# Kernel tuning notes

Measured on AMD Instinct MI355X. Metric: run time of the kernel, lower is better.

## Reference

```python
import jax, jax.numpy as jnp
import numpy as np

N_NODES = 50000
N_EDGES = 600000
IN_DIM = 128
OUT_DIM = 1024


def setup_inputs() -> dict:
    key = jax.random.key(0)
    k1, k2, k3 = jax.random.split(key, 3)
    x = jax.random.normal(k1, (N_NODES, IN_DIM), dtype=jnp.float32)
    edge_index = jax.random.randint(k2, (2, N_EDGES), 0, N_NODES, dtype=jnp.int64)
    # Linear(3*in_dim, out_dim): weight stored as [3*in_dim, out_dim] for x @ W
    W = jax.random.normal(k3, (3 * IN_DIM, OUT_DIM), dtype=jnp.float32) * (1.0 / np.sqrt(3 * IN_DIM))
    b = jnp.zeros((OUT_DIM,), dtype=jnp.float32)
    return {"x": x, "edge_index": edge_index, "W": W, "b": b}


def _mean_aggregate(feats, seg_ids, n):
    # segment-mean: sum gathered features per segment, divide by count (>=1)
    s = jax.ops.segment_sum(feats, seg_ids, num_segments=n)          # [N, d]
    cnt = jax.ops.segment_sum(jnp.ones((feats.shape[0],), feats.dtype), seg_ids, num_segments=n)
    return s / jnp.maximum(cnt, 1.0)[:, None]


def reference(x, edge_index, W, b):
    n = x.shape[0]
    src = edge_index[0]
    dst = edge_index[1]
    # mean over in-neighbors (messages flow src -> dst)
    mean_in = _mean_aggregate(x[src], dst, n)
    # mean over out-neighbors (messages flow dst -> src)
    mean_out = _mean_aggregate(x[dst], src, n)
    h = jnp.concatenate([x, mean_in, mean_out], axis=-1)             # [N, 3*in_dim]
    return jax.nn.relu(h @ W + b)                                    # [N, out_dim]
```

## Files before the change

kernel.cpp:

```cpp
#include <hip/hip_runtime.h>
#include <hip/hip_bf16.h>


typedef __attribute__((ext_vector_type(8))) short bf16x8;
typedef __attribute__((ext_vector_type(4))) short bf16x4;
typedef __attribute__((ext_vector_type(4))) float f32x4;

#define IN_DIM 128
#define AGG 256
#define K3 384
#define ODIM 1024

static __device__ inline short bfs(float f) {
    union { __hip_bfloat16 b; short s; } u;
    u.b = __float2bfloat16(f);
    return u.s;
}

static __device__ inline float bf2f(short s) {
    union { unsigned u; float f; } c;
    c.u = ((unsigned)(unsigned short)s) << 16;
    return c.f;
}

__global__ __launch_bounds__(256) void sage_prep(
    const float* __restrict__ x, const int* __restrict__ src,
    const int* __restrict__ dst, const float* __restrict__ W,
    __hip_bfloat16* __restrict__ xb, __hip_bfloat16* __restrict__ Wt,
    int* __restrict__ deg, int* __restrict__ pos,
    int n_nodes, int n_edges, int wtB, int convB)
{
    int b = blockIdx.x;
    int t = threadIdx.x;
    if (b < wtB) {
        __shared__ __hip_bfloat16 lds[32][36];
        int tk = b / 32, tn = b % 32;
        int k0 = tk * 32, n0 = tn * 32;
        int r = t >> 3, c = (t & 7) * 4;
        f32x4 w = *(const f32x4*)(W + (size_t)(k0 + r) * ODIM + n0 + c);
#pragma unroll
        for (int i = 0; i < 4; ++i) lds[c + i][r] = __float2bfloat16(w[i]);
        __syncthreads();
        *(bf16x4*)&Wt[(size_t)(n0 + r) * K3 + k0 + c] = *(bf16x4*)&lds[r][c];
        return;
    }
    b -= wtB;
    if (b < convB) {
        int tid = b * 256 + t;
        if (tid >= n_nodes * 16) return;
        int i = tid >> 4, d8 = (tid & 15) << 3;
        const float* xp = x + (size_t)i * IN_DIM + d8;
        f32x4 a = *(const f32x4*)xp;
        f32x4 c4 = *(const f32x4*)(xp + 4);
        bf16x8 v;
        v[0] = bfs(a.x); v[1] = bfs(a.y); v[2] = bfs(a.z); v[3] = bfs(a.w);
        v[4] = bfs(c4.x); v[5] = bfs(c4.y); v[6] = bfs(c4.z); v[7] = bfs(c4.w);
        *(bf16x8*)(xb + (size_t)i * IN_DIM + d8) = v;
        return;
    }
    b -= convB;
    int e = b * 256 + t;
    if (e >= 2 * n_edges) return;
    int idx = (e < n_edges) ? dst[e] : n_nodes + src[e - n_edges];
    pos[e] = atomicAdd(deg + idx, 1);
}

__global__ __launch_bounds__(256) void scan_partial(
    const int* __restrict__ deg, int* __restrict__ off, int* __restrict__ bsum, int n)
{
    __shared__ int s[256];
    int t = threadIdx.x;
    int base = blockIdx.x * 1024 + t * 4;
    int4 v = {0, 0, 0, 0};
    if (base + 3 < n) v = *(const int4*)(deg + base);
    else {
        if (base     < n) v.x = deg[base];
        if (base + 1 < n) v.y = deg[base + 1];
        if (base + 2 < n) v.z = deg[base + 2];
        if (base + 3 < n) v.w = deg[base + 3];
    }
    int tsum = v.x + v.y + v.z + v.w;
    s[t] = tsum;
    __syncthreads();
#pragma unroll
    for (int d = 1; d < 256; d <<= 1) {
        int add = (t >= d) ? s[t - d] : 0;
        __syncthreads();
        s[t] += add;
        __syncthreads();
    }
    int excl = s[t] - tsum;
    if (t == 255) bsum[blockIdx.x] = s[255];
    int e0 = excl, e1 = e0 + v.x, e2 = e1 + v.y, e3 = e2 + v.z;
    if (base     < n) off[base]     = e0;
    if (base + 1 < n) off[base + 1] = e1;
    if (base + 2 < n) off[base + 2] = e2;
    if (base + 3 < n) off[base + 3] = e3;
}

__global__ __launch_bounds__(256) void scan_add(
    int* __restrict__ off, const int* __restrict__ bsum, int n, int nblk)
{
    __shared__ int s[256];
    int t = threadIdx.x;
    int v = (t < nblk) ? bsum[t] : 0;
    s[t] = v;
    __syncthreads();
#pragma unroll
    for (int d = 1; d < 256; d <<= 1) {
        int add = (t >= d) ? s[t - d] : 0;
        __syncthreads();
        s[t] += add;
        __syncthreads();
    }
    int b = s[blockIdx.x] - ((blockIdx.x < nblk) ? bsum[blockIdx.x] : 0);
    int base = blockIdx.x * 1024 + t * 4;
#pragma unroll
    for (int j = 0; j < 4; ++j)
        if (base + j < n) off[base + j] += b;
}

__global__ __launch_bounds__(256) void sage_fill(
    const int* __restrict__ src, const int* __restrict__ dst,
    const int* __restrict__ off, const int* __restrict__ pos,
    int* __restrict__ csr, int n_nodes, int n_edges)
{
    int t = blockIdx.x * 256 + threadIdx.x;
    if (t >= 2 * n_edges) return;
    int node, val;
    if (t < n_edges) { node = dst[t]; val = src[t]; }
    else { int e = t - n_edges; node = n_nodes + src[e]; val = dst[e]; }
    csr[off[node] + pos[t]] = val;
}

__global__ __launch_bounds__(256) void sage_aggregate(
    const __hip_bfloat16* __restrict__ xb, const int* __restrict__ csr,
    const int* __restrict__ off, const int* __restrict__ deg,
    __hip_bfloat16* __restrict__ hagg, int n_nodes)
{
    int wid  = (int)((blockIdx.x * 256 + threadIdx.x) >> 6);
    int lane = threadIdx.x & 63;
    if (wid >= 2 * n_nodes) return;
    int i = wid >> 1;
    int d = wid & 1;
    int idx = i + d * n_nodes;

    int b0 = off[idx], dg = deg[idx];
    const int* cp = csr + b0;
    int q = lane >> 4, sub = lane & 15;

    float acc[8];
#pragma unroll
    for (int j = 0; j < 8; ++j) acc[j] = 0.f;

#define ACC8(v) { _Pragma("unroll") \
    for (int j = 0; j < 8; ++j) acc[j] += bf2f((v)[j]); }

    int e = 0;
    for (; e + 7 < dg; e += 8) {
        int r0 = cp[e + q];
        int r1 = cp[e + 4 + q];
        bf16x8 v0 = *(const bf16x8*)(xb + (size_t)r0 * IN_DIM + sub * 8);
        bf16x8 v1 = *(const bf16x8*)(xb + (size_t)r1 * IN_DIM + sub * 8);
        ACC8(v0) ACC8(v1)
    }
    for (; e < dg; e += 4) {
        int eq = e + q;
        int rq = cp[min(eq, dg - 1)];
        bf16x8 v = *(const bf16x8*)(xb + (size_t)rq * IN_DIM + sub * 8);
        if (eq < dg) ACC8(v)
    }
#undef ACC8

#pragma unroll
    for (int j = 0; j < 8; ++j) {
        acc[j] += __shfl_xor(acc[j], 16);
        acc[j] += __shfl_xor(acc[j], 32);
    }

    float inv = 1.0f / (float)max(dg, 1);
    if (q == 0) {
        bf16x8 o;
#pragma unroll
        for (int j = 0; j < 8; ++j) o[j] = bfs(acc[j] * inv);
        *(bf16x8*)(hagg + (size_t)i * AGG + d * IN_DIM + sub * 8) = o;
    }
}

__global__ __launch_bounds__(256, 4) void sage_gemm(
    const __hip_bfloat16* __restrict__ xb, const __hip_bfloat16* __restrict__ hagg,
    const __hip_bfloat16* __restrict__ Wt, const float* __restrict__ bias,
    float* __restrict__ out, int n_nodes)
{
    __shared__ __hip_bfloat16 Asm[2][128 * 32];
    __shared__ __hip_bfloat16 Bsm[2][128 * 32];

    int t    = threadIdx.x;
    int wave = t >> 6;
    int lane = t & 63;

    int bid = blockIdx.x;
    int sid = bid;
    if ((gridDim.x & 7) == 0) {
        int cpx = gridDim.x >> 3;
        sid = (bid & 7) * cpx + (bid >> 3);
    }
    int tn   = sid & 7;
    int tm   = sid >> 3;
    int m0   = tm * 128;
    int n0   = tn * 128;
    int wm   = wave >> 1;
    int wn   = wave & 1;
    int m    = lane & 15;
    int quad = lane >> 4;

    int srow = t >> 2;
    int seg  = t & 3;
    int g    = seg ^ (srow & 3);
    int ga0  = m0 + srow;       if (ga0 >= n_nodes) ga0 = n_nodes - 1;
    int ga1  = m0 + srow + 64;  if (ga1 >= n_nodes) ga1 = n_nodes - 1;
    const __hip_bfloat16* xA0 = xb   + (size_t)ga0 * IN_DIM + g * 8;
    const __hip_bfloat16* xA1 = xb   + (size_t)ga1 * IN_DIM + g * 8;
    const __hip_bfloat16* hA0 = hagg + (size_t)ga0 * AGG    + g * 8;
    const __hip_bfloat16* hA1 = hagg + (size_t)ga1 * AGG    + g * 8;
    const __hip_bfloat16* gB0 = Wt + (size_t)(n0 + srow) * K3 + g * 8;
    const __hip_bfloat16* gB1 = Wt + (size_t)(n0 + srow + 64) * K3 + g * 8;
    int l0 = (0 * 256 + wave * 64) * 8;
    int l1 = (1 * 256 + wave * 64) * 8;

    f32x4 acc[4][4];
#pragma unroll
    for (int s = 0; s < 4; ++s)
#pragma unroll
        for (int u = 0; u < 4; ++u) acc[s][u] = (f32x4){0.f, 0.f, 0.f, 0.f};

    __builtin_amdgcn_global_load_lds(xA0, &Asm[0][l0], 16, 0, 0);
    __builtin_amdgcn_global_load_lds(xA1, &Asm[0][l1], 16, 0, 0);
    __builtin_amdgcn_global_load_lds(gB0, &Bsm[0][l0], 16, 0, 0);
    __builtin_amdgcn_global_load_lds(gB1, &Bsm[0][l1], 16, 0, 0);

    int slot = quad ^ (m & 3);
#pragma unroll
    for (int kt = 0; kt < 12; ++kt) {
        int p = kt & 1;
        __syncthreads();
        if (kt < 11) {
            int kn = kt + 1;
            const __hip_bfloat16* pA0 = (kn < 4) ? xA0 + kn * 32 : hA0 + (kn - 4) * 32;
            const __hip_bfloat16* pA1 = (kn < 4) ? xA1 + kn * 32 : hA1 + (kn - 4) * 32;
            __builtin_amdgcn_global_load_lds(pA0, &Asm[p ^ 1][l0], 16, 0, 0);
            __builtin_amdgcn_global_load_lds(pA1, &Asm[p ^ 1][l1], 16, 0, 0);
            __builtin_amdgcn_global_load_lds(gB0 + kn * 32, &Bsm[p ^ 1][l0], 16, 0, 0);
            __builtin_amdgcn_global_load_lds(gB1 + kn * 32, &Bsm[p ^ 1][l1], 16, 0, 0);
        }
        bf16x8 a[4], b[4];
#pragma unroll
        for (int s = 0; s < 4; ++s) {
            int row = wm * 64 + s * 16 + m;
            a[s] = *(const bf16x8*)&Asm[p][row * 32 + slot * 8];
        }
#pragma unroll
        for (int u = 0; u < 4; ++u) {
            int row = wn * 64 + u * 16 + m;
            b[u] = *(const bf16x8*)&Bsm[p][row * 32 + slot * 8];
        }
#pragma unroll
        for (int s = 0; s < 4; ++s)
#pragma unroll
            for (int u = 0; u < 4; ++u)
                acc[s][u] = __builtin_amdgcn_mfma_f32_16x16x32_bf16(a[s], b[u], acc[s][u], 0, 0, 0);
    }

    float bv[4];
#pragma unroll
    for (int u = 0; u < 4; ++u) bv[u] = bias[n0 + wn * 64 + u * 16 + m];

    bool full = (m0 + 128 <= n_nodes);
    if (full) {
#pragma unroll
        for (int s = 0; s < 4; ++s) {
            int r0 = m0 + wm * 64 + s * 16 + quad * 4;
#pragma unroll
            for (int r = 0; r < 4; ++r) {
                float* orow = out + (size_t)(r0 + r) * ODIM + n0 + wn * 64 + m;
#pragma unroll
                for (int u = 0; u < 4; ++u)
                    __builtin_nontemporal_store(fmaxf(acc[s][u][r] + bv[u], 0.f), orow + u * 16);
            }
        }
    } else {
#pragma unroll
        for (int s = 0; s < 4; ++s) {
            int r0 = m0 + wm * 64 + s * 16 + quad * 4;
#pragma unroll
            for (int r = 0; r < 4; ++r) {
                if (r0 + r >= n_nodes) continue;
                float* orow = out + (size_t)(r0 + r) * ODIM + n0 + wn * 64 + m;
#pragma unroll
                for (int u = 0; u < 4; ++u)
                    __builtin_nontemporal_store(fmaxf(acc[s][u][r] + bv[u], 0.f), orow + u * 16);
            }
        }
    }
}

extern "C" void kernel_launch(void* const* d_in, const int* in_sizes, int n_in,
                              void* d_out, int out_size, void* d_ws, size_t ws_size,
                              hipStream_t stream)
{
    const float* x    = (const float*)d_in[0];
    const int*   ei   = (const int*)d_in[1];
    const float* W    = (const float*)d_in[2];
    const float* bias = (const float*)d_in[3];

    int n_nodes = in_sizes[0] / IN_DIM;
    int n_edges = in_sizes[1] / 2;
    const int* src = ei;
    const int* dst = ei + n_edges;
    int n2 = 2 * n_nodes;

    char* ws = (char*)d_ws;
    int* deg  = (int*)ws;
    int* off  = deg + n2;
    int* bsum = off + n2;
    int* pos  = bsum + 256;
    int* csr  = pos + 2 * n_edges;
    __hip_bfloat16* hagg = (__hip_bfloat16*)(csr + 2 * n_edges);
    __hip_bfloat16* Wt   = hagg + (size_t)n_nodes * AGG;
    __hip_bfloat16* xb   = Wt + (size_t)K3 * ODIM;

    hipMemsetAsync(deg, 0, (size_t)n2 * sizeof(int), stream);

    int wtB   = (K3 / 32) * (ODIM / 32);
    int convB = (n_nodes * 16 + 255) / 256;
    int degB  = (2 * n_edges + 255) / 256;
    sage_prep<<<wtB + convB + degB, 256, 0, stream>>>(
        x, src, dst, W, xb, Wt, deg, pos, n_nodes, n_edges, wtB, convB);

    int nblk = (n2 + 1023) / 1024;
    scan_partial<<<nblk, 256, 0, stream>>>(deg, off, bsum, n2);
    scan_add<<<nblk, 256, 0, stream>>>(off, bsum, n2, nblk);

    sage_fill<<<degB, 256, 0, stream>>>(src, dst, off, pos, csr, n_nodes, n_edges);

    sage_aggregate<<<(n2 + 3) / 4, 256, 0, stream>>>(xb, csr, off, deg, hagg, n_nodes);

    int tiles_m = (n_nodes + 127) / 128;
    int blocks  = tiles_m * (ODIM / 128);
    sage_gemm<<<blocks, 256, 0, stream>>>(xb, hagg, Wt, bias, (float*)d_out, n_nodes);
}
```

Measured before the change: 397.7 us.

## Fuse CSR build stages into one cooperative kernel with grid syncs

Replaces the memset, prep, two scan kernels and fill kernel with a single cooperative persistent kernel of 1024 blocks that uses grid-wide syncs between phases. The goal is to remove several kernel launch gaps and the separate memset. In exchange, the grid-stride loops run fewer blocks than before, and each grid.sync has its own cost. Occupancy is limited by the cooperative launch and the launch bounds.

```diff
diff --git a/kernel.cpp b/kernel.cpp
--- a/kernel.cpp
+++ b/kernel.cpp
@@ -1,5 +1,8 @@
 #include <hip/hip_runtime.h>
 #include <hip/hip_bf16.h>
+#include <hip/hip_cooperative_groups.h>
+
+namespace cg = cooperative_groups;
 
 
 typedef __attribute__((ext_vector_type(8))) short bf16x8;
@@ -10,6 +13,7 @@
 #define AGG 256
 #define K3 384
 #define ODIM 1024
+#define MEGA_NB 1024
 
 static __device__ inline short bfs(float f) {
     union { __hip_bfloat16 b; short s; } u;
@@ -23,114 +27,117 @@
     return c.f;
 }
 
-__global__ __launch_bounds__(256) void sage_prep(
+__global__ __launch_bounds__(256, 4) void sage_mega(
     const float* __restrict__ x, const int* __restrict__ src,
     const int* __restrict__ dst, const float* __restrict__ W,
     __hip_bfloat16* __restrict__ xb, __hip_bfloat16* __restrict__ Wt,
-    int* __restrict__ deg, int* __restrict__ pos,
-    int n_nodes, int n_edges, int wtB, int convB)
+    int* __restrict__ deg, int* __restrict__ pos, int* __restrict__ off,
+    int* __restrict__ bsum, int* __restrict__ csr,
+    int n_nodes, int n_edges, int wtB, int convB, int nblk)
 {
-    int b = blockIdx.x;
-    int t = threadIdx.x;
-    if (b < wtB) {
-        __shared__ __hip_bfloat16 lds[32][36];
-        int tk = b / 32, tn = b % 32;
-        int k0 = tk * 32, n0 = tn * 32;
-        int r = t >> 3, c = (t & 7) * 4;
-        f32x4 w = *(const f32x4*)(W + (size_t)(k0 + r) * ODIM + n0 + c);
-#pragma unroll
-        for (int i = 0; i < 4; ++i) lds[c + i][r] = __float2bfloat16(w[i]);
-        __syncthreads();
-        *(bf16x4*)&Wt[(size_t)(n0 + r) * K3 + k0 + c] = *(bf16x4*)&lds[r][c];
-        return;
-    }
-    b -= wtB;
-    if (b < convB) {
-        int tid = b * 256 + t;
-        if (tid >= n_nodes * 16) return;
-        int i = tid >> 4, d8 = (tid & 15) << 3;
-        const float* xp = x + (size_t)i * IN_DIM + d8;
-        f32x4 a = *(const f32x4*)xp;
-        f32x4 c4 = *(const f32x4*)(xp + 4);
-        bf16x8 v;
-        v[0] = bfs(a.x); v[1] = bfs(a.y); v[2] = bfs(a.z); v[3] = bfs(a.w);
-        v[4] = bfs(c4.x); v[5] = bfs(c4.y); v[6] = bfs(c4.z); v[7] = bfs(c4.w);
-        *(bf16x8*)(xb + (size_t)i * IN_DIM + d8) = v;
-        return;
-    }
-    b -= convB;
-    int e = b * 256 + t;
-    if (e >= 2 * n_edges) return;
-    int idx = (e < n_edges) ? dst[e] : n_nodes + src[e - n_edges];
-    pos[e] = atomicAdd(deg + idx, 1);
-}
-
-__global__ __launch_bounds__(256) void scan_partial(
-    const int* __restrict__ deg, int* __restrict__ off, int* __restrict__ bsum, int n)
-{
-    __shared__ int s[256];
-    int t = threadIdx.x;
-    int base = blockIdx.x * 1024 + t * 4;
-    int4 v = {0, 0, 0, 0};
-    if (base + 3 < n) v = *(const int4*)(deg + base);
-    else {
-        if (base     < n) v.x = deg[base];
-        if (base + 1 < n) v.y = deg[base + 1];
-        if (base + 2 < n) v.z = deg[base + 2];
-        if (base + 3 < n) v.w = deg[base + 3];
-    }
-    int tsum = v.x + v.y + v.z + v.w;
-    s[t] = tsum;
-    __syncthreads();
-#pragma unroll
-    for (int d = 1; d < 256; d <<= 1) {
-        int add = (t >= d) ? s[t - d] : 0;
-        __syncthreads();
-        s[t] += add;
-        __syncthreads();
-    }
-    int excl = s[t] - tsum;
-    if (t == 255) bsum[blockIdx.x] = s[255];
-    int e0 = excl, e1 = e0 + v.x, e2 = e1 + v.y, e3 = e2 + v.z;
-    if (base     < n) off[base]     = e0;
-    if (base + 1 < n) off[base + 1] = e1;
-    if (base + 2 < n) off[base + 2] = e2;
-    if (base + 3 < n) off[base + 3] = e3;
-}
-
-__global__ __launch_bounds__(256) void scan_add(
-    int* __restrict__ off, const int* __restrict__ bsum, int n, int nblk)
-{
-    __shared__ int s[256];
-    int t = threadIdx.x;
-    int v = (t < nblk) ? bsum[t] : 0;
-    s[t] = v;
-    __syncthreads();
-#pragma unroll
-    for (int d = 1; d < 256; d <<= 1) {
-        int add = (t >= d) ? s[t - d] : 0;
-        __syncthreads();
-        s[t] += add;
-        __syncthreads();
-    }
-    int b = s[blockIdx.x] - ((blockIdx.x < nblk) ? bsum[blockIdx.x] : 0);
-    int base = blockIdx.x * 1024 + t * 4;
-#pragma unroll
-    for (int j = 0; j < 4; ++j)
-        if (base + j < n) off[base + j] += b;
-}
-
-__global__ __launch_bounds__(256) void sage_fill(
-    const int* __restrict__ src, const int* __restrict__ dst,
-    const int* __restrict__ off, const int* __restrict__ pos,
-    int* __restrict__ csr, int n_nodes, int n_edges)
-{
-    int t = blockIdx.x * 256 + threadIdx.x;
-    if (t >= 2 * n_edges) return;
-    int node, val;
-    if (t < n_edges) { node = dst[t]; val = src[t]; }
-    else { int e = t - n_edges; node = n_nodes + src[e]; val = dst[e]; }
-    csr[off[node] + pos[t]] = val;
+    cg::grid_group grid = cg::this_grid();
+    __shared__ short wtl[32][36];
+    __shared__ int ss[256];
+    const int NB = (int)gridDim.x;
+    const int t  = threadIdx.x;
+    const int n2 = 2 * n_nodes;
+    const int E2 = 2 * n_edges;
+
+    for (int i = blockIdx.x * 256 + t; i < n2; i += NB * 256) deg[i] = 0;
+    grid.sync();
+
+    int degB = (E2 + 255) >> 8;
+    int totB = wtB + convB + degB;
+    for (int j = blockIdx.x; j < totB; j += NB) {
+        if (j < wtB) {
+            int tk = j / 32, tn = j - tk * 32;
+            int k0 = tk * 32, n0 = tn * 32;
+            int r = t >> 3, c = (t & 7) * 4;
+            f32x4 w = *(const f32x4*)(W + (size_t)(k0 + r) * ODIM + n0 + c);
+#pragma unroll
+            for (int i2 = 0; i2 < 4; ++i2) wtl[c + i2][r] = bfs(w[i2]);
+            __syncthreads();
+            *(bf16x4*)&Wt[(size_t)(n0 + r) * K3 + k0 + c] = *(bf16x4*)&wtl[r][c];
+            __syncthreads();
+        } else if (j < wtB + convB) {
+            int tid = (j - wtB) * 256 + t;
+            if (tid < n_nodes * 16) {
+                int i = tid >> 4, d8 = (tid & 15) << 3;
+                const float* xp = x + (size_t)i * IN_DIM + d8;
+                f32x4 a = *(const f32x4*)xp;
+                f32x4 c4 = *(const f32x4*)(xp + 4);
+                bf16x8 v;
+                v[0] = bfs(a.x); v[1] = bfs(a.y); v[2] = bfs(a.z); v[3] = bfs(a.w);
+                v[4] = bfs(c4.x); v[5] = bfs(c4.y); v[6] = bfs(c4.z); v[7] = bfs(c4.w);
+                *(bf16x8*)(xb + (size_t)i * IN_DIM + d8) = v;
+            }
+        } else {
+            int e = (j - wtB - convB) * 256 + t;
+            if (e < E2) {
+                int idx = (e < n_edges) ? dst[e] : n_nodes + src[e - n_edges];
+                pos[e] = atomicAdd(deg + idx, 1);
+            }
+        }
+    }
+    grid.sync();
+
+    for (int j = blockIdx.x; j < nblk; j += NB) {
+        int base = j * 1024 + t * 4;
+        int4 v = {0, 0, 0, 0};
+        if (base + 3 < n2) v = *(const int4*)(deg + base);
+        else {
+            if (base     < n2) v.x = deg[base];
+            if (base + 1 < n2) v.y = deg[base + 1];
+            if (base + 2 < n2) v.z = deg[base + 2];
+            if (base + 3 < n2) v.w = deg[base + 3];
+        }
+        int tsum = v.x + v.y + v.z + v.w;
+        ss[t] = tsum;
+        __syncthreads();
+#pragma unroll
+        for (int d = 1; d < 256; d <<= 1) {
+            int add = (t >= d) ? ss[t - d] : 0;
+            __syncthreads();
+            ss[t] += add;
+            __syncthreads();
+        }
+        int excl = ss[t] - tsum;
+        if (t == 255) bsum[j] = ss[255];
+        int e0 = excl, e1 = e0 + v.x, e2 = e1 + v.y, e3 = e2 + v.z;
+        if (base     < n2) off[base]     = e0;
+        if (base + 1 < n2) off[base + 1] = e1;
+        if (base + 2 < n2) off[base + 2] = e2;
+        if (base + 3 < n2) off[base + 3] = e3;
+        __syncthreads();
+    }
+    grid.sync();
+
+    for (int j = blockIdx.x; j < nblk; j += NB) {
+        int v = (t < nblk) ? bsum[t] : 0;
+        ss[t] = v;
+        __syncthreads();
+#pragma unroll
+        for (int d = 1; d < 256; d <<= 1) {
+            int add = (t >= d) ? ss[t - d] : 0;
+            __syncthreads();
+            ss[t] += add;
+            __syncthreads();
+        }
+        int boff = ss[j] - bsum[j];
+        int base = j * 1024 + t * 4;
+#pragma unroll
+        for (int jj = 0; jj < 4; ++jj)
+            if (base + jj < n2) off[base + jj] += boff;
+        __syncthreads();
+    }
+    grid.sync();
+
+    for (int e = blockIdx.x * 256 + t; e < E2; e += NB * 256) {
+        int node, val;
+        if (e < n_edges) { node = dst[e]; val = src[e]; }
+        else { int e2 = e - n_edges; node = n_nodes + src[e2]; val = dst[e2]; }
+        csr[off[node] + pos[e]] = val;
+    }
 }
 
 __global__ __launch_bounds__(256) void sage_aggregate(
@@ -329,19 +336,16 @@
     __hip_bfloat16* Wt   = hagg + (size_t)n_nodes * AGG;
     __hip_bfloat16* xb   = Wt + (size_t)K3 * ODIM;
 
-    hipMemsetAsync(deg, 0, (size_t)n2 * sizeof(int), stream);
-
     int wtB   = (K3 / 32) * (ODIM / 32);
     int convB = (n_nodes * 16 + 255) / 256;
-    int degB  = (2 * n_edges + 255) / 256;
-    sage_prep<<<wtB + convB + degB, 256, 0, stream>>>(
-        x, src, dst, W, xb, Wt, deg, pos, n_nodes, n_edges, wtB, convB);
-
-    int nblk = (n2 + 1023) / 1024;
-    scan_partial<<<nblk, 256, 0, stream>>>(deg, off, bsum, n2);
-    scan_add<<<nblk, 256, 0, stream>>>(off, bsum, n2, nblk);
-
-    sage_fill<<<degB, 256, 0, stream>>>(src, dst, off, pos, csr, n_nodes, n_edges);
+    int nblk  = (n2 + 1023) / 1024;
+
+    void* margs[] = {
+        (void*)&x, (void*)&src, (void*)&dst, (void*)&W, (void*)&xb, (void*)&Wt,
+        (void*)&deg, (void*)&pos, (void*)&off, (void*)&bsum, (void*)&csr,
+        (void*)&n_nodes, (void*)&n_edges, (void*)&wtB, (void*)&convB, (void*)&nblk
+    };
+    hipLaunchCooperativeKernel(sage_mega, dim3(MEGA_NB), dim3(256), margs, 0, stream);
 
     sage_aggregate<<<(n2 + 3) / 4, 256, 0, stream>>>(xb, csr, off, deg, hagg, n_nodes);
 
```

Result: slower. 769.3 us (+93.4%).

## Keep full-K weight slice resident in LDS and stream A fragments from global

Applied to the files above, without the earlier changes.

The GEMM tile changes from 128x128 to 256x64. The whole 64x384 weight slice is loaded once into swizzled LDS, and each wave reads its A fragments directly from global memory into registers. This drops the per-K-step double-buffered LDS staging and the per-iteration barriers. In exchange, A loads become uncoalesced 16-byte per-lane global reads with no prefetch, and each block uses 48KB of LDS, which may limit occupancy.

```diff
diff --git a/kernel.cpp b/kernel.cpp
--- a/kernel.cpp
+++ b/kernel.cpp
@@ -192,8 +192,7 @@
     const __hip_bfloat16* __restrict__ Wt, const float* __restrict__ bias,
     float* __restrict__ out, int n_nodes)
 {
-    __shared__ __hip_bfloat16 Asm[2][128 * 32];
-    __shared__ __hip_bfloat16 Bsm[2][128 * 32];
+    __shared__ __hip_bfloat16 Bl[64 * K3];
 
     int t    = threadIdx.x;
     int wave = t >> 6;
@@ -205,28 +204,32 @@
         int cpx = gridDim.x >> 3;
         sid = (bid & 7) * cpx + (bid >> 3);
     }
-    int tn   = sid & 7;
-    int tm   = sid >> 3;
-    int m0   = tm * 128;
-    int n0   = tn * 128;
-    int wm   = wave >> 1;
-    int wn   = wave & 1;
+    int tn = sid & 15;
+    int tm = sid >> 4;
+    int m0 = tm * 256;
+    int n0 = tn * 64;
     int m    = lane & 15;
     int quad = lane >> 4;
 
-    int srow = t >> 2;
-    int seg  = t & 3;
-    int g    = seg ^ (srow & 3);
-    int ga0  = m0 + srow;       if (ga0 >= n_nodes) ga0 = n_nodes - 1;
-    int ga1  = m0 + srow + 64;  if (ga1 >= n_nodes) ga1 = n_nodes - 1;
-    const __hip_bfloat16* xA0 = xb   + (size_t)ga0 * IN_DIM + g * 8;
-    const __hip_bfloat16* xA1 = xb   + (size_t)ga1 * IN_DIM + g * 8;
-    const __hip_bfloat16* hA0 = hagg + (size_t)ga0 * AGG    + g * 8;
-    const __hip_bfloat16* hA1 = hagg + (size_t)ga1 * AGG    + g * 8;
-    const __hip_bfloat16* gB0 = Wt + (size_t)(n0 + srow) * K3 + g * 8;
-    const __hip_bfloat16* gB1 = Wt + (size_t)(n0 + srow + 64) * K3 + g * 8;
-    int l0 = (0 * 256 + wave * 64) * 8;
-    int l1 = (1 * 256 + wave * 64) * 8;
+    const __hip_bfloat16* WtS = Wt + (size_t)n0 * K3;
+#pragma unroll
+    for (int r = 0; r < 12; ++r) {
+        int le  = (r * 256 + t) * 8;
+        int row = le / K3;
+        int off = le - row * K3;
+        int srco = row * K3 + (off ^ ((row & 7) << 3));
+        __builtin_amdgcn_global_load_lds(WtS + srco, &Bl[(r * 256 + wave * 64) * 8], 16, 0, 0);
+    }
+
+    const __hip_bfloat16* ax[4];
+    const __hip_bfloat16* ah[4];
+#pragma unroll
+    for (int s = 0; s < 4; ++s) {
+        int row = m0 + wave * 64 + s * 16 + m;
+        if (row >= n_nodes) row = n_nodes - 1;
+        ax[s] = xb   + (size_t)row * IN_DIM + quad * 8;
+        ah[s] = hagg + (size_t)row * AGG    + quad * 8;
+    }
 
     f32x4 acc[4][4];
 #pragma unroll
@@ -234,35 +237,20 @@
 #pragma unroll
         for (int u = 0; u < 4; ++u) acc[s][u] = (f32x4){0.f, 0.f, 0.f, 0.f};
 
-    __builtin_amdgcn_global_load_lds(xA0, &Asm[0][l0], 16, 0, 0);
-    __builtin_amdgcn_global_load_lds(xA1, &Asm[0][l1], 16, 0, 0);
-    __builtin_amdgcn_global_load_lds(gB0, &Bsm[0][l0], 16, 0, 0);
-    __builtin_amdgcn_global_load_lds(gB1, &Bsm[0][l1], 16, 0, 0);
-
-    int slot = quad ^ (m & 3);
+    __syncthreads();
+
 #pragma unroll
     for (int kt = 0; kt < 12; ++kt) {
-        int p = kt & 1;
-        __syncthreads();
-        if (kt < 11) {
-            int kn = kt + 1;
-            const __hip_bfloat16* pA0 = (kn < 4) ? xA0 + kn * 32 : hA0 + (kn - 4) * 32;
-            const __hip_bfloat16* pA1 = (kn < 4) ? xA1 + kn * 32 : hA1 + (kn - 4) * 32;
-            __builtin_amdgcn_global_load_lds(pA0, &Asm[p ^ 1][l0], 16, 0, 0);
-            __builtin_amdgcn_global_load_lds(pA1, &Asm[p ^ 1][l1], 16, 0, 0);
-            __builtin_amdgcn_global_load_lds(gB0 + kn * 32, &Bsm[p ^ 1][l0], 16, 0, 0);
-            __builtin_amdgcn_global_load_lds(gB1 + kn * 32, &Bsm[p ^ 1][l1], 16, 0, 0);
-        }
         bf16x8 a[4], b[4];
 #pragma unroll
-        for (int s = 0; s < 4; ++s) {
-            int row = wm * 64 + s * 16 + m;
-            a[s] = *(const bf16x8*)&Asm[p][row * 32 + slot * 8];
-        }
+        for (int s = 0; s < 4; ++s)
+            a[s] = (kt < 4) ? *(const bf16x8*)(ax[s] + kt * 32)
+                            : *(const bf16x8*)(ah[s] + (kt - 4) * 32);
 #pragma unroll
         for (int u = 0; u < 4; ++u) {
-            int row = wn * 64 + u * 16 + m;
-            b[u] = *(const bf16x8*)&Bsm[p][row * 32 + slot * 8];
+            int row  = u * 16 + m;
+            int koff = (kt * 32 + quad * 8) ^ ((row & 7) << 3);
+            b[u] = *(const bf16x8*)&Bl[row * K3 + koff];
         }
 #pragma unroll
         for (int s = 0; s < 4; ++s)
@@ -273,16 +261,16 @@
 
     float bv[4];
 #pragma unroll
-    for (int u = 0; u < 4; ++u) bv[u] = bias[n0 + wn * 64 + u * 16 + m];
-
-    bool full = (m0 + 128 <= n_nodes);
+    for (int u = 0; u < 4; ++u) bv[u] = bias[n0 + u * 16 + m];
+
+    bool full = (m0 + 256 <= n_nodes);
     if (full) {
 #pragma unroll
         for (int s = 0; s < 4; ++s) {
-            int r0 = m0 + wm * 64 + s * 16 + quad * 4;
+            int r0 = m0 + wave * 64 + s * 16 + quad * 4;
 #pragma unroll
             for (int r = 0; r < 4; ++r) {
-                float* orow = out + (size_t)(r0 + r) * ODIM + n0 + wn * 64 + m;
+                float* orow = out + (size_t)(r0 + r) * ODIM + n0 + m;
 #pragma unroll
                 for (int u = 0; u < 4; ++u)
                     __builtin_nontemporal_store(fmaxf(acc[s][u][r] + bv[u], 0.f), orow + u * 16);
@@ -291,11 +279,11 @@
     } else {
 #pragma unroll
         for (int s = 0; s < 4; ++s) {
-            int r0 = m0 + wm * 64 + s * 16 + quad * 4;
+            int r0 = m0 + wave * 64 + s * 16 + quad * 4;
 #pragma unroll
             for (int r = 0; r < 4; ++r) {
                 if (r0 + r >= n_nodes) continue;
-                float* orow = out + (size_t)(r0 + r) * ODIM + n0 + wn * 64 + m;
+                float* orow = out + (size_t)(r0 + r) * ODIM + n0 + m;
 #pragma unroll
                 for (int u = 0; u < 4; ++u)
                     __builtin_nontemporal_store(fmaxf(acc[s][u][r] + bv[u], 0.f), orow + u * 16);
@@ -345,7 +333,7 @@
 
     sage_aggregate<<<(n2 + 3) / 4, 256, 0, stream>>>(xb, csr, off, deg, hagg, n_nodes);
 
-    int tiles_m = (n_nodes + 127) / 128;
-    int blocks  = tiles_m * (ODIM / 128);
+    int tiles_m = (n_nodes + 255) / 256;
+    int blocks  = tiles_m * (ODIM / 64);
     sage_gemm<<<blocks, 256, 0, stream>>>(xb, hagg, Wt, bias, (float*)d_out, n_nodes);
 }
```

New measurement: 430.6 us. 1.08x slower.
